# Kernel optimization log

Measured on AMD Instinct MI355X. Metric: run time of the kernel, lower is better.

The kernel has to match this reference:

```python
import jax, jax.numpy as jnp
import numpy as np

B, T, IN, H, OUT = 1024, 512, 16, 64, 8


def setup_inputs() -> dict:
    key = jax.random.key(0)
    ks = jax.random.split(key, 7)
    s = 1.0 / np.sqrt(H)
    return {
        "x": jax.random.normal(ks[0], (B, T, IN), dtype=jnp.float32),
        "W_ih": jax.random.normal(ks[1], (4 * H, IN), dtype=jnp.float32) * s,
        "W_hh": jax.random.normal(ks[2], (4 * H, H), dtype=jnp.float32) * s,
        "b_ih": jax.random.normal(ks[3], (4 * H,), dtype=jnp.float32) * s,
        "b_hh": jax.random.normal(ks[4], (4 * H,), dtype=jnp.float32) * s,
        "W_fc": jax.random.normal(ks[5], (OUT, H), dtype=jnp.float32) * s,
        "b_fc": jax.random.normal(ks[6], (OUT,), dtype=jnp.float32) * s,
    }


def reference(x, W_ih, W_hh, b_ih, b_hh, W_fc, b_fc):
    Bq, Tq, _ = x.shape
    Hq = W_hh.shape[1]
    # Precompute input contribution for all timesteps: [T, B, 4H]
    xw = jnp.einsum("bti,gi->tbg", x, W_ih) + b_ih + b_hh

    def step(carry, xw_t):
        h, c = carry
        gates = xw_t + h @ W_hh.T  # [B, 4H]
        i, f, g, o = jnp.split(gates, 4, axis=-1)  # PyTorch gate order i,f,g,o
        i = jax.nn.sigmoid(i)
        f = jax.nn.sigmoid(f)
        g = jnp.tanh(g)
        o = jax.nn.sigmoid(o)
        c = f * c + i * g
        h = o * jnp.tanh(c)
        return (h, c), None

    h0 = jnp.zeros((Bq, Hq), dtype=x.dtype)
    c0 = jnp.zeros((Bq, Hq), dtype=x.dtype)
    (h_last, _), _ = jax.lax.scan(step, (h0, c0), xw)

    # fc on last timestep only, then sigmoid -> [B, 1, OUT]
    out = jax.nn.sigmoid(h_last @ W_fc.T + b_fc)
    return out[:, None, :]
```

## Files before the change

kernel.cpp:

```cpp
#include <hip/hip_runtime.h>
#include <math.h>


#define LSTM_T 512
#define LSTM_IN 16
#define LSTM_H 64
#define LSTM_OUT 8
#define BT 2
#define HSTRIDE 80
#define XSTR 73
#define XWSZ 2336

#define L2E   1.44269504088896340736f
#define L2E2  2.88539008177792681472f

typedef _Float16 half8  __attribute__((ext_vector_type(8)));
typedef float    floatx4 __attribute__((ext_vector_type(4)));

static __device__ __forceinline__ float fast_rcp(float x) { return __builtin_amdgcn_rcpf(x); }
static __device__ __forceinline__ float fast_exp2(float x) { return __builtin_amdgcn_exp2f(x); }
static __device__ __forceinline__ float sigm2(float p) { return fast_rcp(1.0f + fast_exp2(-p)); }
static __device__ __forceinline__ void pin4(int4& v) {
    asm volatile("" : "+v"(v.x), "+v"(v.y), "+v"(v.z), "+v"(v.w));
}
static __device__ __forceinline__ void pinf4(float4& v) {
    asm volatile("" : "+v"(v.x), "+v"(v.y), "+v"(v.z), "+v"(v.w));
}
static __device__ __forceinline__ void lite_barrier() {
    asm volatile("s_waitcnt lgkmcnt(0)\n\ts_barrier" ::: "memory");
}
static __device__ __forceinline__ unsigned pk2h(float a, float b) {
    return __builtin_bit_cast(unsigned, __builtin_amdgcn_cvt_pkrtz(a, b));
}
static __device__ __forceinline__ half8 to_h8(float4 a, float4 b) {
    uint4 u = make_uint4(pk2h(a.x, a.y), pk2h(a.z, a.w), pk2h(b.x, b.y), pk2h(b.z, b.w));
    return __builtin_bit_cast(half8, u);
}
static __device__ __forceinline__ int4 cvt8h(float4 a, float4 b) {
    return __builtin_bit_cast(int4, to_h8(a, b));
}
static __device__ __forceinline__ float4 ld4(const float* p) {
    return *reinterpret_cast<const float4*>(p);
}
static __device__ __forceinline__ float4 scl4(float4 v, float s) {
    return make_float4(s * v.x, s * v.y, s * v.z, s * v.w);
}
static __device__ __forceinline__ float sel4(floatx4 v, bool r0, bool r1) {
    float lo = r0 ? v[1] : v[0];
    float hi = r0 ? v[3] : v[2];
    return r1 ? hi : lo;
}
static __device__ __forceinline__ float dpp8(float v) {
    int r = __builtin_amdgcn_update_dpp(0, __builtin_bit_cast(int, v),
                                        0x128, 0xF, 0xF, false);
    return __builtin_bit_cast(float, r);
}

#define MF(A_, B_, C_) __builtin_amdgcn_mfma_f32_16x16x32_f16( \
        __builtin_bit_cast(half8, A_), (B_), (C_), 0, 0, 0)
#define B4(i) __builtin_bit_cast(floatx4, bias4[i])

__global__ __launch_bounds__(256, 2)
void lstm_mfma_kernel(const float* __restrict__ x,
                      const float* __restrict__ W_ih,
                      const float* __restrict__ W_hh,
                      const float* __restrict__ b_ih,
                      const float* __restrict__ b_hh,
                      const float* __restrict__ W_fc,
                      const float* __restrict__ b_fc,
                      float* __restrict__ out) {
    const int tid   = threadIdx.x;
    const int lane  = tid & 63;
    const int w     = tid >> 6;
    const int q     = lane >> 4;
    const int m     = lane & 15;
    const int b     = m & 1;
    const int dt    = m >> 1;
    const int rho   = (m >> 1) & 3;
    const bool r0   = (rho & 1) != 0;
    const bool r1   = (rho & 2) != 0;
    const bool h1   = (m & 8) != 0;
    const int h1i   = h1 ? 1 : 0;
    const bool wr   = (m < 8);
    const int jmine = 16 * w + 4 * q + rho;
    const int bbase = blockIdx.x * BT;

    const float a1 = h1 ? 1.0f : 0.0f;
    const float b1 = h1 ? -2.0f : 1.0f;

    __shared__ __align__(16)  float2   xwbuf[2][XWSZ];
    __shared__ __align__(128) _Float16 hbuf[2][BT][HSTRIDE];
    __shared__ __align__(16)  float    hfin[BT][LSTM_H];

    int4 Ah[4][2], Ax[4];
    float4 bias4[4];
    #pragma unroll
    for (int tt = 0; tt < 4; ++tt) {
        const float sc = (tt == 2) ? L2E2 : -L2E;
        const int gt = tt * 64 + 16 * w + m;
        #pragma unroll
        for (int c = 0; c < 2; ++c) {
            const float* s = W_hh + gt * LSTM_H + 32 * c + 8 * q;
            Ah[tt][c] = cvt8h(scl4(ld4(s), sc), scl4(ld4(s + 4), sc));
            pin4(Ah[tt][c]);
        }
        float4 xa = make_float4(0.f, 0.f, 0.f, 0.f), xb = xa;
        if (q < 2) {
            const float* s = W_ih + gt * LSTM_IN + 8 * q;
            xa = ld4(s); xb = ld4(s + 4);
        }
        Ax[tt] = cvt8h(scl4(xa, sc), scl4(xb, sc));
        pin4(Ax[tt]);
        const int gb = tt * 64 + 16 * w + 4 * q;
        float4 bi = ld4(b_ih + gb), bh = ld4(b_hh + gb);
        bias4[tt] = make_float4(sc * (bi.x + bh.x), sc * (bi.y + bh.y),
                                sc * (bi.z + bh.z), sc * (bi.w + bh.w));
        pinf4(bias4[tt]);
    }

    float4 zc4 = make_float4(0.f, 0.f, 0.f, 0.f);
    pinf4(zc4);
    const floatx4 zc = __builtin_bit_cast(floatx4, zc4);

    if (tid < 80) reinterpret_cast<int*>(&hbuf[0][0][0])[tid] = 0;

    const float* xpb = x + (size_t)(bbase + b) * LSTM_T * LSTM_IN
                         + (size_t)dt * LSTM_IN + 8 * q;
    float4 Xb0 = make_float4(0.f, 0.f, 0.f, 0.f), Xb1 = Xb0;
    if (q < 2) { Xb0 = ld4(xpb); Xb1 = ld4(xpb + 4); }

    floatx4 aXi_, aXf_, aXg_, aXo_;
    half8 xfb;
    {
        half8 x0 = to_h8(Xb0, Xb1);
        aXi_ = MF(Ax[0], x0, B4(0));
        aXf_ = MF(Ax[1], x0, B4(1));
        aXg_ = MF(Ax[2], x0, B4(2));
        aXo_ = MF(Ax[3], x0, B4(3));
        float2* xwch = &xwbuf[0][0];
        #pragma unroll
        for (int r = 0; r < 4; ++r) {
            int jw = (16 * w + 4 * q + r) ^ dt;
            xwch[(dt * 4 + 2 * b + 0) * XSTR + jw] = make_float2(aXf_[r], aXi_[r]);
            xwch[(dt * 4 + 2 * b + 1) * XSTR + jw] = make_float2(aXg_[r], aXo_[r]);
        }
    }
    if (q < 2) {
        Xb0 = ld4(xpb + 8 * LSTM_IN);
        Xb1 = ld4(xpb + 8 * LSTM_IN + 4);
    }
    __syncthreads();

    float2 xwc = xwbuf[0][(2 * b + h1i) * XSTR + jmine];
    float cs = 0.0f, hreg = 0.0f;

#define STEP_CORE(T_, PK, KN, NCB, ...)                                         \
    {                                                                           \
        const _Float16* cur = &hbuf[PK][0][0];                                  \
        _Float16*       nxt = &hbuf[(PK) ^ 1][0][0];                            \
        half8 bh0 = *reinterpret_cast<const half8*>(cur + b * HSTRIDE + 8 * q); \
        half8 bh1 = *reinterpret_cast<const half8*>(cur + b * HSTRIDE + 32 + 8 * q); \
        __VA_ARGS__                                                             \
                 \
        float2 xwn = xwbuf[NCB][((KN) * 4 + 2 * b + h1i) * XSTR                 \
                                + (jmine ^ (KN))];                              \
                       \
        floatx4 accf = MF(Ah[1][0], bh0, zc);                                   \
        floatx4 accg = MF(Ah[2][0], bh0, zc);                                   \
        floatx4 acci = MF(Ah[0][0], bh0, zc);                                   \
        floatx4 acco = MF(Ah[3][0], bh0, zc);                                   \
        accf = MF(Ah[1][1], bh1, accf);                                         \
        accg = MF(Ah[2][1], bh1, accg);                                         \
        __builtin_amdgcn_s_setprio(1);                                          \
        float uf = sel4(accf, r0, r1);                                          \
        float ug = sel4(accg, r0, r1);                                          \
        float u1 = (h1 ? ug : uf) + xwc.x;                                      \
        float e1 = fast_exp2(u1);                                               \
        acci = MF(Ah[0][1], bh1, acci);                                         \
        acco = MF(Ah[3][1], bh1, acco);                                         \
            \
        float act1 = fmaf(b1, fast_rcp(1.0f + e1), a1);                         \
        float uii = sel4(acci, r0, r1);                                         \
        float uoo = sel4(acco, r0, r1);                                         \
        float u2 = (h1 ? uoo : uii) + xwc.y;                                    \
        float e2 = fast_exp2(u2);                                               \
        float act2 = fast_rcp(1.0f + e2);      \
        float g_in = dpp8(act1);                       \
        float o_in = dpp8(act2);                      \
        float Ki   = L2E2 * act2;                    \
                 \
        cs = fmaf(act1, cs, Ki * g_in);                                         \
        float E  = fast_exp2(cs);                                               \
        float r_ = fast_rcp(1.0f + E);                                          \
        float n2o = -2.0f * o_in;                        \
        hreg = fmaf(n2o, r_, o_in);                           \
        if (wr) nxt[b * HSTRIDE + jmine] = (_Float16)hreg;                      \
        __builtin_amdgcn_s_setprio(0);                                          \
        lite_barrier();                                                         \
        xwc = xwn;                                                              \
    }

#define BWR(WB, PR, R_)                                                         \
    {                                                                           \
        float2* xwch = &xwbuf[WB][0];                                           \
        int jw0 = (16 * w + 4 * q + (R_)) ^ dt;                                 \
        int jw1 = (16 * w + 4 * q + (R_) + 1) ^ dt;                             \
        xwch[(dt * 4 + 2 * b + (PR)) * XSTR + jw0] = (PR)                       \
            ? make_float2(aXg_[(R_)], aXo_[(R_)])                               \
            : make_float2(aXf_[(R_)], aXi_[(R_)]);                              \
        xwch[(dt * 4 + 2 * b + (PR)) * XSTR + jw1] = (PR)                       \
            ? make_float2(aXg_[(R_) + 1], aXo_[(R_) + 1])                       \
            : make_float2(aXf_[(R_) + 1], aXi_[(R_) + 1]);                      \
    }

    for (int t8 = 0; t8 < LSTM_T; t8 += 8) {
        const int cb = (t8 >> 3) & 1;
        const int wb = cb ^ 1;
        const bool dob = t8 < LSTM_T - 8;
        const bool dox = t8 < LSTM_T - 16;
        STEP_CORE(t8 + 0, 0, 1, cb,
            if (dob) { xfb = to_h8(Xb0, Xb1); aXi_ = MF(Ax[0], xfb, B4(0)); })
        STEP_CORE(t8 + 1, 1, 2, cb,
            if (dob) { aXf_ = MF(Ax[1], xfb, B4(1)); })
        STEP_CORE(t8 + 2, 0, 3, cb,
            if (dob) { aXg_ = MF(Ax[2], xfb, B4(2)); })
        STEP_CORE(t8 + 3, 1, 4, cb,
            if (dob) { aXo_ = MF(Ax[3], xfb, B4(3)); })
        STEP_CORE(t8 + 4, 0, 5, cb,
            if (dob) { BWR(wb, 0, 0) })
        STEP_CORE(t8 + 5, 1, 6, cb,
            if (dob) { BWR(wb, 0, 2) })
        STEP_CORE(t8 + 6, 0, 7, cb,
            if (dob) { BWR(wb, 1, 0) }
            if (q < 2 && dox) { Xb0 = ld4(xpb + (size_t)(t8 + 16) * LSTM_IN); })
        STEP_CORE(t8 + 7, 1, 0, wb,
            if (dob) { BWR(wb, 1, 2) }
            if (q < 2 && dox) { Xb1 = ld4(xpb + (size_t)(t8 + 16) * LSTM_IN + 4); })
    }
#undef STEP_CORE
#undef BWR

    if (wr) hfin[b][jmine] = hreg;
    __syncthreads();

    if (tid < BT * LSTM_OUT) {
        int bb = tid >> 3, o = tid & 7;
        float s = b_fc[o];
        #pragma unroll
        for (int j4 = 0; j4 < LSTM_H / 4; ++j4) {
            float4 wv = ld4(W_fc + o * LSTM_H + 4 * j4);
            float4 hv = *reinterpret_cast<const float4*>(&hfin[bb][4 * j4]);
            s = fmaf(wv.x, hv.x, s);
            s = fmaf(wv.y, hv.y, s);
            s = fmaf(wv.z, hv.z, s);
            s = fmaf(wv.w, hv.w, s);
        }
        out[(size_t)(bbase + bb) * LSTM_OUT + o] = sigm2(s * L2E);
    }
}

extern "C" void kernel_launch(void* const* d_in, const int* in_sizes, int n_in,
                              void* d_out, int out_size, void* d_ws, size_t ws_size,
                              hipStream_t stream) {
    const float* x    = (const float*)d_in[0];
    const float* W_ih = (const float*)d_in[1];
    const float* W_hh = (const float*)d_in[2];
    const float* b_ih = (const float*)d_in[3];
    const float* b_hh = (const float*)d_in[4];
    const float* W_fc = (const float*)d_in[5];
    const float* b_fc = (const float*)d_in[6];
    float* out = (float*)d_out;

    lstm_mfma_kernel<<<1024 / BT, 256, 0, stream>>>(
        x, W_ih, W_hh, b_ih, b_hh, W_fc, b_fc, out);
}
```

Measured before the change: 226.5 us.

## Unroll LSTM loop by 16 with precomputed LDS pointers and unconditional h writes

Unrolls the time loop to 16 steps so the xw buffer indices become compile-time constants, and precomputes per-lane LDS pointers so each step uses immediate offsets instead of recomputed addresses. The hbuf gets a second half so lanes that used to skip the write (m>=8) now store to a dummy region, which removes the predicated store branch. The L2E2 scale is folded into the a1/b1 constants, which drops one multiply per step. Code size grows, and the extra dead LDS writes add some LDS traffic.

```diff
diff --git a/kernel.cpp b/kernel.cpp
--- a/kernel.cpp
+++ b/kernel.cpp
@@ -8,6 +8,7 @@
 #define LSTM_OUT 8
 #define BT 2
 #define HSTRIDE 80
+#define HPSTR 320
 #define XSTR 73
 #define XWSZ 2336
 
@@ -85,11 +86,11 @@
     const int jmine = 16 * w + 4 * q + rho;
     const int bbase = blockIdx.x * BT;
 
-    const float a1 = h1 ? 1.0f : 0.0f;
-    const float b1 = h1 ? -2.0f : 1.0f;
+    const float a1 = h1 ? L2E2 : 0.0f;
+    const float b1 = h1 ? (-2.0f * L2E2) : 1.0f;
 
     __shared__ __align__(16)  float2   xwbuf[2][XWSZ];
-    __shared__ __align__(128) _Float16 hbuf[2][BT][HSTRIDE];
+    __shared__ __align__(128) _Float16 hbuf[2][2 * BT][HSTRIDE];
     __shared__ __align__(16)  float    hfin[BT][LSTM_H];
 
     int4 Ah[4][2], Ax[4];
@@ -122,12 +123,34 @@
     pinf4(zc4);
     const floatx4 zc = __builtin_bit_cast(floatx4, zc4);
 
-    if (tid < 80) reinterpret_cast<int*>(&hbuf[0][0][0])[tid] = 0;
+    const float2* xwp[8];
+    #pragma unroll
+    for (int k = 0; k < 8; ++k)
+        xwp[k] = &xwbuf[0][(2 * b + h1i) * XSTR + (jmine ^ k)];
+    float2* xww[2][4];
+    #pragma unroll
+    for (int pr = 0; pr < 2; ++pr)
+        #pragma unroll
+        for (int r = 0; r < 4; ++r)
+            xww[pr][r] = &xwbuf[0][(dt * 4 + 2 * b + pr) * XSTR
+                                   + ((16 * w + 4 * q + r) ^ dt)];
+    const _Float16* hrp = &hbuf[0][b][8 * q];
+    _Float16*       hwp = &hbuf[0][h1 ? 2 + b : b][jmine];
+
+    if (tid < 160) reinterpret_cast<int*>(&hbuf[0][0][0])[tid] = 0;
 
     const float* xpb = x + (size_t)(bbase + b) * LSTM_T * LSTM_IN
                          + (size_t)dt * LSTM_IN + 8 * q;
     float4 Xb0 = make_float4(0.f, 0.f, 0.f, 0.f), Xb1 = Xb0;
     if (q < 2) { Xb0 = ld4(xpb); Xb1 = ld4(xpb + 4); }
+
+#define BWR(WB, PR, R_)                                                         \
+    xww[PR][R_][(WB) * XWSZ] = (PR)                                             \
+        ? make_float2(aXg_[R_], aXo_[R_])                                       \
+        : make_float2(aXf_[R_], aXi_[R_]);                                      \
+    xww[PR][(R_) + 1][(WB) * XWSZ] = (PR)                                       \
+        ? make_float2(aXg_[(R_) + 1], aXo_[(R_) + 1])                           \
+        : make_float2(aXf_[(R_) + 1], aXi_[(R_) + 1]);
 
     floatx4 aXi_, aXf_, aXg_, aXo_;
     half8 xfb;
@@ -137,13 +160,7 @@
         aXf_ = MF(Ax[1], x0, B4(1));
         aXg_ = MF(Ax[2], x0, B4(2));
         aXo_ = MF(Ax[3], x0, B4(3));
-        float2* xwch = &xwbuf[0][0];
-        #pragma unroll
-        for (int r = 0; r < 4; ++r) {
-            int jw = (16 * w + 4 * q + r) ^ dt;
-            xwch[(dt * 4 + 2 * b + 0) * XSTR + jw] = make_float2(aXf_[r], aXi_[r]);
-            xwch[(dt * 4 + 2 * b + 1) * XSTR + jw] = make_float2(aXg_[r], aXo_[r]);
-        }
+        BWR(0, 0, 0) BWR(0, 0, 2) BWR(0, 1, 0) BWR(0, 1, 2)
     }
     if (q < 2) {
         Xb0 = ld4(xpb + 8 * LSTM_IN);
@@ -151,19 +168,16 @@
     }
     __syncthreads();
 
-    float2 xwc = xwbuf[0][(2 * b + h1i) * XSTR + jmine];
+    float2 xwc = xwp[0][0];
     float cs = 0.0f, hreg = 0.0f;
 
-#define STEP_CORE(T_, PK, KN, NCB, ...)                                         \
+#define STEP_CORE(PK, KN, NC, ...)                                              \
     {                                                                           \
-        const _Float16* cur = &hbuf[PK][0][0];                                  \
-        _Float16*       nxt = &hbuf[(PK) ^ 1][0][0];                            \
-        half8 bh0 = *reinterpret_cast<const half8*>(cur + b * HSTRIDE + 8 * q); \
-        half8 bh1 = *reinterpret_cast<const half8*>(cur + b * HSTRIDE + 32 + 8 * q); \
+        half8 bh0 = *reinterpret_cast<const half8*>(hrp + (PK) * HPSTR);        \
+        half8 bh1 = *reinterpret_cast<const half8*>(hrp + (PK) * HPSTR + 32);   \
         __VA_ARGS__                                                             \
-                 \
-        float2 xwn = xwbuf[NCB][((KN) * 4 + 2 * b + h1i) * XSTR                 \
-                                + (jmine ^ (KN))];                              \
+                               \
+        float2 xwn = xwp[KN][(NC) * XWSZ + (KN) * 4 * XSTR];                    \
                        \
         floatx4 accf = MF(Ah[1][0], bh0, zc);                                   \
         floatx4 accg = MF(Ah[2][0], bh0, zc);                                   \
@@ -178,64 +192,51 @@
         float e1 = fast_exp2(u1);                                               \
         acci = MF(Ah[0][1], bh1, acci);                                         \
         acco = MF(Ah[3][1], bh1, acco);                                         \
-            \
+                            \
         float act1 = fmaf(b1, fast_rcp(1.0f + e1), a1);                         \
         float uii = sel4(acci, r0, r1);                                         \
         float uoo = sel4(acco, r0, r1);                                         \
         float u2 = (h1 ? uoo : uii) + xwc.y;                                    \
         float e2 = fast_exp2(u2);                                               \
-        float act2 = fast_rcp(1.0f + e2);      \
-        float g_in = dpp8(act1);                       \
-        float o_in = dpp8(act2);                      \
-        float Ki   = L2E2 * act2;                    \
-                 \
-        cs = fmaf(act1, cs, Ki * g_in);                                         \
+        float act2 = fast_rcp(1.0f + e2);         \
+        float g_in = dpp8(act1);                      \
+        float o_in = dpp8(act2);                          \
+                \
+        cs = fmaf(act1, cs, act2 * g_in);                                       \
         float E  = fast_exp2(cs);                                               \
         float r_ = fast_rcp(1.0f + E);                                          \
         float n2o = -2.0f * o_in;                        \
         hreg = fmaf(n2o, r_, o_in);                           \
-        if (wr) nxt[b * HSTRIDE + jmine] = (_Float16)hreg;                      \
+        hwp[((PK) ^ 1) * HPSTR] = (_Float16)hreg;            \
         __builtin_amdgcn_s_setprio(0);                                          \
         lite_barrier();                                                         \
         xwc = xwn;                                                              \
     }
 
-#define BWR(WB, PR, R_)                                                         \
-    {                                                                           \
-        float2* xwch = &xwbuf[WB][0];                                           \
-        int jw0 = (16 * w + 4 * q + (R_)) ^ dt;                                 \
-        int jw1 = (16 * w + 4 * q + (R_) + 1) ^ dt;                             \
-        xwch[(dt * 4 + 2 * b + (PR)) * XSTR + jw0] = (PR)                       \
-            ? make_float2(aXg_[(R_)], aXo_[(R_)])                               \
-            : make_float2(aXf_[(R_)], aXi_[(R_)]);                              \
-        xwch[(dt * 4 + 2 * b + (PR)) * XSTR + jw1] = (PR)                       \
-            ? make_float2(aXg_[(R_) + 1], aXo_[(R_) + 1])                       \
-            : make_float2(aXf_[(R_) + 1], aXi_[(R_) + 1]);                      \
-    }
-
-    for (int t8 = 0; t8 < LSTM_T; t8 += 8) {
-        const int cb = (t8 >> 3) & 1;
-        const int wb = cb ^ 1;
-        const bool dob = t8 < LSTM_T - 8;
-        const bool dox = t8 < LSTM_T - 16;
-        STEP_CORE(t8 + 0, 0, 1, cb,
-            if (dob) { xfb = to_h8(Xb0, Xb1); aXi_ = MF(Ax[0], xfb, B4(0)); })
-        STEP_CORE(t8 + 1, 1, 2, cb,
-            if (dob) { aXf_ = MF(Ax[1], xfb, B4(1)); })
-        STEP_CORE(t8 + 2, 0, 3, cb,
-            if (dob) { aXg_ = MF(Ax[2], xfb, B4(2)); })
-        STEP_CORE(t8 + 3, 1, 4, cb,
-            if (dob) { aXo_ = MF(Ax[3], xfb, B4(3)); })
-        STEP_CORE(t8 + 4, 0, 5, cb,
-            if (dob) { BWR(wb, 0, 0) })
-        STEP_CORE(t8 + 5, 1, 6, cb,
-            if (dob) { BWR(wb, 0, 2) })
-        STEP_CORE(t8 + 6, 0, 7, cb,
-            if (dob) { BWR(wb, 1, 0) }
-            if (q < 2 && dox) { Xb0 = ld4(xpb + (size_t)(t8 + 16) * LSTM_IN); })
-        STEP_CORE(t8 + 7, 1, 0, wb,
-            if (dob) { BWR(wb, 1, 2) }
-            if (q < 2 && dox) { Xb1 = ld4(xpb + (size_t)(t8 + 16) * LSTM_IN + 4); })
+    for (int t16 = 0; t16 < LSTM_T; t16 += 16) {
+        const bool more = (t16 + 16) < LSTM_T;
+        STEP_CORE(0, 1, 0,
+            { xfb = to_h8(Xb0, Xb1); aXi_ = MF(Ax[0], xfb, B4(0)); })
+        STEP_CORE(1, 2, 0, { aXf_ = MF(Ax[1], xfb, B4(1)); })
+        STEP_CORE(0, 3, 0, { aXg_ = MF(Ax[2], xfb, B4(2)); })
+        STEP_CORE(1, 4, 0, { aXo_ = MF(Ax[3], xfb, B4(3)); })
+        STEP_CORE(0, 5, 0, { BWR(1, 0, 0) })
+        STEP_CORE(1, 6, 0, { BWR(1, 0, 2) })
+        STEP_CORE(0, 7, 0, { BWR(1, 1, 0)
+            if (q < 2 && more) Xb0 = ld4(xpb + (size_t)(t16 + 16) * LSTM_IN); })
+        STEP_CORE(1, 0, 1, { BWR(1, 1, 2)
+            if (q < 2 && more) Xb1 = ld4(xpb + (size_t)(t16 + 16) * LSTM_IN + 4); })
+        STEP_CORE(0, 1, 1,
+            { if (more) { xfb = to_h8(Xb0, Xb1); aXi_ = MF(Ax[0], xfb, B4(0)); } })
+        STEP_CORE(1, 2, 1, { if (more) { aXf_ = MF(Ax[1], xfb, B4(1)); } })
+        STEP_CORE(0, 3, 1, { if (more) { aXg_ = MF(Ax[2], xfb, B4(2)); } })
+        STEP_CORE(1, 4, 1, { if (more) { aXo_ = MF(Ax[3], xfb, B4(3)); } })
+        STEP_CORE(0, 5, 1, { if (more) { BWR(0, 0, 0) } })
+        STEP_CORE(1, 6, 1, { if (more) { BWR(0, 0, 2) } })
+        STEP_CORE(0, 7, 1, { if (more) { BWR(0, 1, 0) }
+            if (q < 2 && more) Xb0 = ld4(xpb + (size_t)(t16 + 24) * LSTM_IN); })
+        STEP_CORE(1, 0, 0, { if (more) { BWR(0, 1, 2) }
+            if (q < 2 && more) Xb1 = ld4(xpb + (size_t)(t16 + 24) * LSTM_IN + 4); })
     }
 #undef STEP_CORE
 #undef BWR
```

Result: no change. 222.2 us (-1.9%).
